# Kernel tuning notes

Measured on AMD Instinct MI355X. Metric: run time of the kernel, lower is better.

## Reference

```python
import jax, jax.numpy as jnp
import numpy as np

R = 256            # rois_per_image = cfg.TRAIN.BATCH_SIZE
FG_QUOTA = 64      # round(FG_FRACTION=0.25 * R)
FG_THRESH = 0.5
BG_HI = 0.5
BG_LO = 0.0
MEANS = jnp.array([0.0, 0.0, 0.0, 0.0], jnp.float32)
STDS = jnp.array([0.1, 0.1, 0.2, 0.2], jnp.float32)
INSIDE_W = jnp.array([1.0, 1.0, 1.0, 1.0], jnp.float32)


def _iou(boxes, gt):
    # boxes [B,M,4], gt [B,G,4] -> IoU [B,M,G]  (bbox_overlaps_batch2)
    x1 = jnp.maximum(boxes[:, :, None, 0], gt[:, None, :, 0])
    y1 = jnp.maximum(boxes[:, :, None, 1], gt[:, None, :, 1])
    x2 = jnp.minimum(boxes[:, :, None, 2], gt[:, None, :, 2])
    y2 = jnp.minimum(boxes[:, :, None, 3], gt[:, None, :, 3])
    iw = jnp.clip(x2 - x1 + 1.0, 0.0)
    ih = jnp.clip(y2 - y1 + 1.0, 0.0)
    inter = iw * ih
    area_b = (boxes[..., 2] - boxes[..., 0] + 1.0) * (boxes[..., 3] - boxes[..., 1] + 1.0)
    area_g = (gt[..., 2] - gt[..., 0] + 1.0) * (gt[..., 3] - gt[..., 1] + 1.0)
    return inter / (area_b[:, :, None] + area_g[:, None, :] - inter)


def _bbox_transform(ex, gt):
    # bbox_transform_batch2: ex,gt [B,R,4] -> targets [B,R,4]
    ew = ex[..., 2] - ex[..., 0] + 1.0
    eh = ex[..., 3] - ex[..., 1] + 1.0
    ecx = ex[..., 0] + 0.5 * ew
    ecy = ex[..., 1] + 0.5 * eh
    gw = gt[..., 2] - gt[..., 0] + 1.0
    gh = gt[..., 3] - gt[..., 1] + 1.0
    gcx = gt[..., 0] + 0.5 * gw
    gcy = gt[..., 1] + 0.5 * gh
    return jnp.stack([(gcx - ecx) / ew, (gcy - ecy) / eh,
                      jnp.log(gw / ew), jnp.log(gh / eh)], axis=-1)


def setup_inputs() -> dict:
    key = jax.random.key(0)
    B, N, G, IMG = 16, 12000, 128, 800.0
    ks = jax.random.split(key, 8)

    def boxes(k1, k2, n):
        xy = jax.random.uniform(k1, (B, n, 2)) * (IMG - 260.0)
        wh = 16.0 + jax.random.uniform(k2, (B, n, 2)) * 240.0
        return jnp.concatenate([xy, xy + wh], axis=-1)

    roi_xy = boxes(ks[0], ks[1], N)
    bidx = jnp.broadcast_to(jnp.arange(B, dtype=jnp.float32)[:, None, None], (B, N, 1))
    all_rois = jnp.concatenate([bidx, roi_xy], axis=-1)  # [B,N,5]

    gt_xy = boxes(ks[2], ks[3], G)
    gt_lab = jax.random.randint(ks[4], (B, G, 1), 1, 151).astype(jnp.float32)
    gt_boxes = jnp.concatenate([gt_xy, gt_lab], axis=-1)  # [B,G,5]
    return {"all_rois": all_rois, "gt_boxes": gt_boxes}


def reference(all_rois, gt_boxes):
    B, N, _ = all_rois.shape
    G = gt_boxes.shape[1]
    bidx = jnp.arange(B, dtype=all_rois.dtype)

    # append gt boxes as extra proposals (first col = image index)
    gt_append = jnp.concatenate(
        [jnp.broadcast_to(bidx[:, None, None], (B, G, 1)), gt_boxes[:, :, :4]], axis=2)
    rois_all = jnp.concatenate([all_rois, gt_append], axis=1)  # [B,M,5], M=N+G

    ov = _iou(rois_all[..., 1:5], gt_boxes[..., :4])  # [B,M,G]
    max_ov = ov.max(axis=2)
    gt_asgn = ov.argmax(axis=2)
    labels = jnp.take_along_axis(gt_boxes[..., 4], gt_asgn, axis=1)  # [B,M]

    fg_mask = max_ov >= FG_THRESH
    bg_mask = (max_ov < BG_HI) & (max_ov >= BG_LO)

    # deterministic random sampling via keyed top_k (replaces np.random.permutation)
    k1, k2 = jax.random.split(jax.random.key(42))
    r1 = jax.random.uniform(k1, max_ov.shape)
    r2 = jax.random.uniform(k2, max_ov.shape)
    _, fg_top = jax.lax.top_k(jnp.where(fg_mask, r1 + 2.0, r1), R)  # fg first, randomized
    _, bg_top = jax.lax.top_k(jnp.where(bg_mask, r2 + 2.0, r2), R)

    fg_num = fg_mask.sum(axis=1)
    bg_num = bg_mask.sum(axis=1)
    fg_count = jnp.minimum(fg_num, FG_QUOTA)[:, None]          # [B,1]
    bg_avail = jnp.clip(bg_num, 1, R)[:, None]
    pos = jnp.broadcast_to(jnp.arange(R)[None, :], (B, R))

    fg_pick = jnp.take_along_axis(fg_top, jnp.minimum(pos, jnp.maximum(fg_count - 1, 0)), axis=1)
    bg_pick = jnp.take_along_axis(bg_top, (pos - fg_count) % bg_avail, axis=1)
    keep = jnp.where(pos < fg_count, fg_pick, bg_pick)         # [B,R]

    lab = jnp.take_along_axis(labels, keep, axis=1)
    lab = jnp.where(pos < fg_count, lab, 0.0)                  # bg -> class 0

    rois = jnp.take_along_axis(rois_all, keep[..., None], axis=1)  # [B,R,5]
    rois = rois.at[..., 0].set(bidx[:, None])

    asgn = jnp.take_along_axis(gt_asgn, keep, axis=1)
    gt_sel = jnp.take_along_axis(gt_boxes[..., :4], asgn[..., None], axis=1)

    t = (_bbox_transform(rois[..., 1:5], gt_sel) - MEANS) / STDS
    fg4 = (lab > 0).astype(t.dtype)[..., None]
    bbox_targets = t * fg4
    inside_w = fg4 * INSIDE_W
    outside_w = (inside_w > 0).astype(t.dtype)
    return rois, lab, bbox_targets, inside_w, outside_w
```

## Files before the change

### kernel.cpp

```cpp
#include <hip/hip_runtime.h>
#include <cstdint>
#include <cstddef>


#define THREEFRY_PARTITIONABLE 1

constexpr int kB = 16;
constexpr int kN = 12000;
constexpr int kG = 128;
constexpr int kM = kN + kG;
constexpr int kM4 = kM / 4;
constexpr int kR = 256;
constexpr int kFgQuota = 64;
constexpr unsigned kSeedHi = 0u;
constexpr unsigned kSeedLo = 42u;

__device__ __forceinline__ int imin(int a, int b) { return a < b ? a : b; }
__device__ __forceinline__ int imax(int a, int b) { return a > b ? a : b; }

__device__ __forceinline__ unsigned rotl32(unsigned v, int d) {
  return (v << d) | (v >> (32 - d));
}

__device__ __forceinline__ void tf2x32(unsigned k0, unsigned k1,
                                       unsigned x0, unsigned x1,
                                       unsigned& o0, unsigned& o1) {
  const unsigned k2 = k0 ^ k1 ^ 0x1BD11BDAu;
  x0 += k0; x1 += k1;
#define TF_R(d) x0 += x1; x1 = rotl32(x1, d); x1 ^= x0;
  TF_R(13) TF_R(15) TF_R(26) TF_R(6)
  x0 += k1; x1 += k2 + 1u;
  TF_R(17) TF_R(29) TF_R(16) TF_R(24)
  x0 += k2; x1 += k0 + 2u;
  TF_R(13) TF_R(15) TF_R(26) TF_R(6)
  x0 += k0; x1 += k1 + 3u;
  TF_R(17) TF_R(29) TF_R(16) TF_R(24)
  x0 += k1; x1 += k2 + 4u;
  TF_R(13) TF_R(15) TF_R(26) TF_R(6)
  x0 += k2; x1 += k0 + 5u;
#undef TF_R
  o0 = x0; o1 = x1;
}

__device__ __forceinline__ void derive_key(int which, unsigned& ka, unsigned& kb) {
#if THREEFRY_PARTITIONABLE
  tf2x32(kSeedHi, kSeedLo, 0u, (unsigned)which, ka, kb);
#else
  unsigned a0, a1, b0, b1;
  tf2x32(kSeedHi, kSeedLo, 0u, 2u, a0, a1);
  tf2x32(kSeedHi, kSeedLo, 1u, 3u, b0, b1);
  if (which == 0) { ka = a0; kb = b0; } else { ka = a1; kb = b1; }
#endif
}

__device__ __forceinline__ float bits_to_uniform(unsigned bits) {
  return __uint_as_float((bits >> 9) | 0x3f800000u) - 1.0f;
}

__device__ __forceinline__ float jax_uniform(unsigned ka, unsigned kb, unsigned i) {
#if THREEFRY_PARTITIONABLE
  unsigned o0, o1;
  tf2x32(ka, kb, 0u, i, o0, o1);
  return bits_to_uniform(o0 ^ o1);
#else
  const unsigned H = (unsigned)(kB * kM) / 2u;
  unsigned o0, o1;
  if (i < H) { tf2x32(ka, kb, i, i + H, o0, o1); return bits_to_uniform(o0); }
  else       { tf2x32(ka, kb, i - H, i, o0, o1); return bits_to_uniform(o1); }
#endif
}

__device__ __forceinline__ unsigned mask_bin(unsigned v) {
  unsigned bn = (v - 0x40000000u) >> 11;
  return bn > 2047u ? 2047u : bn;
}

__global__ __launch_bounds__(256) void k_prep(const float* __restrict__ all_rois,
                                              const float* __restrict__ gt_boxes,
                                              unsigned* __restrict__ vb) {
  __shared__ float4 sg[kG];
  __shared__ float sga[kG];
  const int b = blockIdx.y;
  const int tid = threadIdx.x;
  if (tid < kG) {
    const float* gp = gt_boxes + ((size_t)b * kG + tid) * 5;
    const float x0 = gp[0], y0 = gp[1], x1 = gp[2], y1 = gp[3];
    sg[tid] = make_float4(x0, y0, x1, y1);
    sga[tid] = ((x1 - x0) + 1.0f) * ((y1 - y0) + 1.0f);
  }
  __syncthreads();

  const int m = blockIdx.x * 256 + tid;
  if (m >= kM) return;

  float bx0, by0, bx1, by1;
  if (m < kN) {
    const float* rp = all_rois + ((size_t)b * kN + m) * 5;
    bx0 = rp[1]; by0 = rp[2]; bx1 = rp[3]; by1 = rp[4];
  } else {
    const float4 g4 = sg[m - kN];
    bx0 = g4.x; by0 = g4.y; bx1 = g4.z; by1 = g4.w;
  }
  const float areab = ((bx1 - bx0) + 1.0f) * ((by1 - by0) + 1.0f);

  int fg = 0;
#pragma unroll 4
  for (int g = 0; g < kG; ++g) {
    const float4 g4 = sg[g];
    const float xx0 = fmaxf(bx0, g4.x);
    const float yy0 = fmaxf(by0, g4.y);
    const float xx1 = fminf(bx1, g4.z);
    const float yy1 = fminf(by1, g4.w);
    const float iw = fmaxf((xx1 - xx0) + 1.0f, 0.0f);
    const float ih = fmaxf((yy1 - yy0) + 1.0f, 0.0f);
    const float inter = iw * ih;
    const float denom = (areab + sga[g]) - inter;
    fg |= (__builtin_fmaf(-0.5f, denom, inter) >= (-0x1p-26f) * denom) ? 1 : 0;
  }

  unsigned k1a, k1b, k2a, k2b;
  derive_key(0, k1a, k1b);
  derive_key(1, k2a, k2b);
  const unsigned i = (unsigned)(b * kM + m);
  const float r1 = jax_uniform(k1a, k1b, i);
  const float r2 = jax_uniform(k2a, k2b, i);
  const float v1 = fg ? (r1 + 2.0f) : r1;
  const float v2 = fg ? r2 : (r2 + 2.0f);
  vb[(size_t)b * kM + m] = __float_as_uint(v1);
  vb[(size_t)(kB + b) * kM + m] = __float_as_uint(v2);
}

__device__ __forceinline__ int block_reduce_sum(int v, int* s_red, int tid) {
#pragma unroll
  for (int off = 32; off > 0; off >>= 1) v += __shfl_down(v, off, 64);
  __syncthreads();
  if ((tid & 63) == 0) s_red[tid >> 6] = v;
  __syncthreads();
  return s_red[0] + s_red[1] + s_red[2] + s_red[3];
}

__global__ __launch_bounds__(256) void k_select(const unsigned* __restrict__ vb,
                                                int* __restrict__ topidx,
                                                int* __restrict__ nin) {
  __shared__ int s_hist[2048];
  __shared__ unsigned long long s_cand[1024];
  __shared__ int s_scan[256];
  __shared__ int s_red[4];
  __shared__ unsigned long long s_wmax[4];
  __shared__ int s_tbin, s_cnt;

  const int which = blockIdx.x;
  const int b = blockIdx.y;
  const int tid = threadIdx.x;
  const unsigned* src = vb + (size_t)(which * kB + b) * kM;
  const uint4* src4 = (const uint4*)src;
  int* dst = topidx + (size_t)(which * kB + b) * kR;

  for (int i = tid; i < 2048; i += 256) s_hist[i] = 0;
  if (tid == 0) s_cnt = 0;
  __syncthreads();

#pragma unroll 4
  for (int i = tid; i < kM4; i += 256) {
    const uint4 u = src4[i];
#define HBIN(x) if ((x) >= 0x40000000u) atomicAdd(&s_hist[mask_bin(x)], 1);
    HBIN(u.x) HBIN(u.y) HBIN(u.z) HBIN(u.w)
#undef HBIN
  }
  __syncthreads();

  const int base = 2048 - 8 * (tid + 1);
  int s = 0;
#pragma unroll
  for (int j = 0; j < 8; ++j) s += s_hist[base + j];
  const int n_in = block_reduce_sum(s, s_red, tid);
  if (tid == 0) nin[which * kB + b] = n_in;
  const int quota = (which == 0) ? kFgQuota : kR;
  const int K = imin(n_in, quota);

  if (K == 0) {
    if (which == 0) return;
    unsigned long long best = 0ull;
    for (int m = tid; m < kM; m += 256) {
      const unsigned long long key =
          ((unsigned long long)src[m] << 32) | (unsigned)(0xFFFFFFFFu - (unsigned)m);
      if (key > best) best = key;
    }
#pragma unroll
    for (int off = 32; off > 0; off >>= 1) {
      const unsigned long long o = __shfl_down(best, off, 64);
      if (o > best) best = o;
    }
    if ((tid & 63) == 0) s_wmax[tid >> 6] = best;
    __syncthreads();
    if (tid == 0) {
      for (int w = 1; w < 4; ++w) if (s_wmax[w] > best) best = s_wmax[w];
      dst[0] = (int)(0xFFFFFFFFu - (unsigned)(best & 0xFFFFFFFFull));
    }
    return;
  }

  s_scan[tid] = s;
  __syncthreads();
  for (int off = 1; off < 256; off <<= 1) {
    const int add = (tid >= off) ? s_scan[tid - off] : 0;
    __syncthreads();
    s_scan[tid] += add;
    __syncthreads();
  }
  const int above = s_scan[tid] - s;
  int cum = above;
  for (int j = 7; j >= 0; --j) {
    const int c = s_hist[base + j];
    if (cum < K && cum + c >= K) s_tbin = base + j;
    cum += c;
  }
  __syncthreads();
  const unsigned tbin = (unsigned)s_tbin;

#pragma unroll 4
  for (int i = tid; i < kM4; i += 256) {
    const uint4 u = src4[i];
#define CAND(x, j)                                                         \
    if ((x) >= 0x40000000u && mask_bin(x) >= tbin) {                       \
      const int p = atomicAdd(&s_cnt, 1);                                  \
      if (p < 1024)                                                        \
        s_cand[p] = ((unsigned long long)(x) << 32) |                      \
                    (unsigned)(0xFFFFFFFFu - (unsigned)(4 * i + (j)));     \
    }
    CAND(u.x, 0) CAND(u.y, 1) CAND(u.z, 2) CAND(u.w, 3)
#undef CAND
  }
  __syncthreads();
  const int Nc = imin(s_cnt, 1024);

  for (int j = tid; j < Nc; j += 256) {
    const unsigned long long key = s_cand[j];
    int rank = 0;
    for (int i = 0; i < Nc; ++i) rank += (s_cand[i] > key) ? 1 : 0;
    if (rank < K)
      dst[rank] = (int)(0xFFFFFFFFu - (unsigned)(key & 0xFFFFFFFFull));
  }
}

__global__ __launch_bounds__(256) void k_final(const float* __restrict__ all_rois,
                                               const float* __restrict__ gt_boxes,
                                               const int* __restrict__ topidx,
                                               const int* __restrict__ nin,
                                               float* __restrict__ out) {
  const int lane = threadIdx.x & 63;
  const int idx = (blockIdx.x << 2) | (threadIdx.x >> 6);
  const int b = idx >> 8;
  const int pos = idx & 255;

  const int fgc = imin(nin[b], kFgQuota);
  const int bgav = imin(imax(nin[kB + b], 1), kR);
  const bool isfg = pos < fgc;
  int keep;
  if (isfg) keep = topidx[(size_t)b * kR + imin(pos, imax(fgc - 1, 0))];
  else      keep = topidx[(size_t)(kB + b) * kR + (pos - fgc) % bgav];

  const float* bp = (keep < kN) ? (all_rois + ((size_t)b * kN + keep) * 5 + 1)
                                : (gt_boxes + ((size_t)b * kG + (keep - kN)) * 5);
  const float bx0 = bp[0], by0 = bp[1], bx1 = bp[2], by1 = bp[3];
  const float areab = ((bx1 - bx0) + 1.0f) * ((by1 - by0) + 1.0f);

  unsigned long long best = 0ull;
#pragma unroll
  for (int h = 0; h < 2; ++h) {
    const int g = lane + 64 * h;
    const float* gp = gt_boxes + ((size_t)b * kG + g) * 5;
    const float gx0 = gp[0], gy0 = gp[1], gx1 = gp[2], gy1 = gp[3];
    const float ga = ((gx1 - gx0) + 1.0f) * ((gy1 - gy0) + 1.0f);
    const float xx0 = fmaxf(bx0, gx0);
    const float yy0 = fmaxf(by0, gy0);
    const float xx1 = fminf(bx1, gx1);
    const float yy1 = fminf(by1, gy1);
    const float iw = fmaxf((xx1 - xx0) + 1.0f, 0.0f);
    const float ih = fmaxf((yy1 - yy0) + 1.0f, 0.0f);
    const float inter = iw * ih;
    const float iou = inter / ((areab + ga) - inter);
    const unsigned long long key =
        ((unsigned long long)__float_as_uint(iou) << 7) | (unsigned)(127 - g);
    if (key > best) best = key;
  }
#pragma unroll
  for (int off = 1; off < 64; off <<= 1) {
    const unsigned long long o = __shfl_xor(best, off, 64);
    if (o > best) best = o;
  }
  const int a = 127 - (int)(best & 127ull);

  const float* gp = gt_boxes + ((size_t)b * kG + a) * 5;
  const float gx0 = gp[0], gy0 = gp[1], gx1 = gp[2], gy1 = gp[3];
  const float lab = isfg ? gp[4] : 0.0f;
  const float fg4 = (lab > 0.0f) ? 1.0f : 0.0f;

  const float ew = (bx1 - bx0) + 1.0f;
  const float eh = (by1 - by0) + 1.0f;
  const float ecx = bx0 + 0.5f * ew;
  const float ecy = by0 + 0.5f * eh;
  const float gw = (gx1 - gx0) + 1.0f;
  const float gh = (gy1 - gy0) + 1.0f;
  const float gcx = gx0 + 0.5f * gw;
  const float gcy = gy0 + 0.5f * gh;
  const float t0 = ((gcx - ecx) / ew) / 0.1f;
  const float t1 = ((gcy - ecy) / eh) / 0.1f;
  const float t2 = logf(gw / ew) / 0.2f;
  const float t3 = logf(gh / eh) / 0.2f;

  if (lane == 0) {
    float* o_rois = out;
    float* o_lab  = out + (size_t)kB * kR * 5;
    float* o_tgt  = o_lab + (size_t)kB * kR;
    float* o_iw   = o_tgt + (size_t)kB * kR * 4;
    float* o_ow   = o_iw  + (size_t)kB * kR * 4;
    const size_t p = (size_t)b * kR + pos;
    o_rois[p * 5 + 0] = (float)b;
    o_rois[p * 5 + 1] = bx0;
    o_rois[p * 5 + 2] = by0;
    o_rois[p * 5 + 3] = bx1;
    o_rois[p * 5 + 4] = by1;
    o_lab[p] = lab;
    o_tgt[p * 4 + 0] = t0 * fg4;
    o_tgt[p * 4 + 1] = t1 * fg4;
    o_tgt[p * 4 + 2] = t2 * fg4;
    o_tgt[p * 4 + 3] = t3 * fg4;
    o_iw[p * 4 + 0] = fg4; o_iw[p * 4 + 1] = fg4;
    o_iw[p * 4 + 2] = fg4; o_iw[p * 4 + 3] = fg4;
    o_ow[p * 4 + 0] = fg4; o_ow[p * 4 + 1] = fg4;
    o_ow[p * 4 + 2] = fg4; o_ow[p * 4 + 3] = fg4;
  }
}

extern "C" void kernel_launch(void* const* d_in, const int* in_sizes, int n_in_args,
                              void* d_out, int out_size, void* d_ws, size_t ws_size,
                              hipStream_t stream) {
  (void)in_sizes; (void)n_in_args; (void)out_size; (void)ws_size;
  const float* all_rois = (const float*)d_in[0];
  const float* gt_boxes = (const float*)d_in[1];
  float* out = (float*)d_out;

  char* ws = (char*)d_ws;
  unsigned* vb = (unsigned*)ws;
  int* topidx  = (int*)(ws + 1572864);
  int* nin     = (int*)(ws + 1572864 + 32768);

  dim3 gA((kM + 255) / 256, kB);
  k_prep<<<gA, 256, 0, stream>>>(all_rois, gt_boxes, vb);
  dim3 gB(2, kB);
  k_select<<<gB, 256, 0, stream>>>(vb, topidx, nin);
  k_final<<<1024, 256, 0, stream>>>(all_rois, gt_boxes, topidx, nin, out);
}
```

Measured before the change: 99.47 us.

## Split IoU loop across thread halves and widen select blocks to 1024 threads

k_prep now gives each ROI two threads, each testing half of the 128 GT boxes, combines the fg flag through shared memory, and has each half produce one of the two random streams. This doubles the grid and halves the per-thread serial work. k_select grows from 256 to 1024 threads per block so the histogram, candidate and rank passes over each row finish in fewer iterations, since only 32 blocks run. The cost is extra barriers, a shared-memory exchange, and more idle threads in the scan stage. derive_key is also rewritten to compute both keys and select one.

```diff
diff --git a/kernel.cpp b/kernel.cpp
--- a/kernel.cpp
+++ b/kernel.cpp
@@ -44,12 +44,17 @@
 
 __device__ __forceinline__ void derive_key(int which, unsigned& ka, unsigned& kb) {
 #if THREEFRY_PARTITIONABLE
-  tf2x32(kSeedHi, kSeedLo, 0u, (unsigned)which, ka, kb);
+  unsigned a0, a1, b0, b1;
+  tf2x32(kSeedHi, kSeedLo, 0u, 0u, a0, a1);
+  tf2x32(kSeedHi, kSeedLo, 0u, 1u, b0, b1);
+  ka = which ? b0 : a0;
+  kb = which ? b1 : a1;
 #else
   unsigned a0, a1, b0, b1;
   tf2x32(kSeedHi, kSeedLo, 0u, 2u, a0, a1);
   tf2x32(kSeedHi, kSeedLo, 1u, 3u, b0, b1);
-  if (which == 0) { ka = a0; kb = b0; } else { ka = a1; kb = b1; }
+  ka = which ? a1 : a0;
+  kb = which ? b1 : b0;
 #endif
 }
 
@@ -80,6 +85,7 @@
                                               unsigned* __restrict__ vb) {
   __shared__ float4 sg[kG];
   __shared__ float sga[kG];
+  __shared__ int s_fgp[2][128];
   const int b = blockIdx.y;
   const int tid = threadIdx.x;
   if (tid < kG) {
@@ -88,24 +94,29 @@
     sg[tid] = make_float4(x0, y0, x1, y1);
     sga[tid] = ((x1 - x0) + 1.0f) * ((y1 - y0) + 1.0f);
   }
-  __syncthreads();
-
-  const int m = blockIdx.x * 256 + tid;
-  if (m >= kM) return;
-
-  float bx0, by0, bx1, by1;
-  if (m < kN) {
-    const float* rp = all_rois + ((size_t)b * kN + m) * 5;
-    bx0 = rp[1]; by0 = rp[2]; bx1 = rp[3]; by1 = rp[4];
-  } else {
-    const float4 g4 = sg[m - kN];
-    bx0 = g4.x; by0 = g4.y; bx1 = g4.z; by1 = g4.w;
+  const int rl = tid & 127;
+  const int h = tid >> 7;
+  const int m = blockIdx.x * 128 + rl;
+  const bool valid = (m < kM);
+  __syncthreads();
+
+  float bx0 = 0.f, by0 = 0.f, bx1 = 0.f, by1 = 0.f;
+  if (valid) {
+    if (m < kN) {
+      const float* rp = all_rois + ((size_t)b * kN + m) * 5;
+      bx0 = rp[1]; by0 = rp[2]; bx1 = rp[3]; by1 = rp[4];
+    } else {
+      const float4 g4 = sg[m - kN];
+      bx0 = g4.x; by0 = g4.y; bx1 = g4.z; by1 = g4.w;
+    }
   }
   const float areab = ((bx1 - bx0) + 1.0f) * ((by1 - by0) + 1.0f);
 
-  int fg = 0;
-#pragma unroll 4
-  for (int g = 0; g < kG; ++g) {
+  int fgp = 0;
+  const int g0 = h * 64;
+#pragma unroll 8
+  for (int gg = 0; gg < 64; ++gg) {
+    const int g = g0 + gg;
     const float4 g4 = sg[g];
     const float xx0 = fmaxf(bx0, g4.x);
     const float yy0 = fmaxf(by0, g4.y);
@@ -115,38 +126,40 @@
     const float ih = fmaxf((yy1 - yy0) + 1.0f, 0.0f);
     const float inter = iw * ih;
     const float denom = (areab + sga[g]) - inter;
-    fg |= (__builtin_fmaf(-0.5f, denom, inter) >= (-0x1p-26f) * denom) ? 1 : 0;
-  }
-
-  unsigned k1a, k1b, k2a, k2b;
-  derive_key(0, k1a, k1b);
-  derive_key(1, k2a, k2b);
+    fgp |= (__builtin_fmaf(-0.5f, denom, inter) >= (-0x1p-26f) * denom) ? 1 : 0;
+  }
+  s_fgp[h][rl] = fgp;
+  __syncthreads();
+  if (!valid) return;
+  const int fg = s_fgp[0][rl] | s_fgp[1][rl];
+
+  unsigned ka, kb;
+  derive_key(h, ka, kb);
   const unsigned i = (unsigned)(b * kM + m);
-  const float r1 = jax_uniform(k1a, k1b, i);
-  const float r2 = jax_uniform(k2a, k2b, i);
-  const float v1 = fg ? (r1 + 2.0f) : r1;
-  const float v2 = fg ? r2 : (r2 + 2.0f);
-  vb[(size_t)b * kM + m] = __float_as_uint(v1);
-  vb[(size_t)(kB + b) * kM + m] = __float_as_uint(v2);
-}
-
-__device__ __forceinline__ int block_reduce_sum(int v, int* s_red, int tid) {
+  const float r = jax_uniform(ka, kb, i);
+  const float v = (fg ^ h) ? (r + 2.0f) : r;
+  vb[(size_t)(h * kB + b) * kM + m] = __float_as_uint(v);
+}
+
+__device__ __forceinline__ int block_reduce_sum_w(int v, int* s_red, int tid, int nw) {
 #pragma unroll
   for (int off = 32; off > 0; off >>= 1) v += __shfl_down(v, off, 64);
   __syncthreads();
   if ((tid & 63) == 0) s_red[tid >> 6] = v;
   __syncthreads();
-  return s_red[0] + s_red[1] + s_red[2] + s_red[3];
-}
-
-__global__ __launch_bounds__(256) void k_select(const unsigned* __restrict__ vb,
-                                                int* __restrict__ topidx,
-                                                int* __restrict__ nin) {
+  int t = 0;
+  for (int w = 0; w < nw; ++w) t += s_red[w];
+  return t;
+}
+
+__global__ __launch_bounds__(1024) void k_select(const unsigned* __restrict__ vb,
+                                                 int* __restrict__ topidx,
+                                                 int* __restrict__ nin) {
   __shared__ int s_hist[2048];
   __shared__ unsigned long long s_cand[1024];
   __shared__ int s_scan[256];
-  __shared__ int s_red[4];
-  __shared__ unsigned long long s_wmax[4];
+  __shared__ int s_red[16];
+  __shared__ unsigned long long s_wmax[16];
   __shared__ int s_tbin, s_cnt;
 
   const int which = blockIdx.x;
@@ -156,12 +169,11 @@
   const uint4* src4 = (const uint4*)src;
   int* dst = topidx + (size_t)(which * kB + b) * kR;
 
-  for (int i = tid; i < 2048; i += 256) s_hist[i] = 0;
+  for (int i = tid; i < 2048; i += 1024) s_hist[i] = 0;
   if (tid == 0) s_cnt = 0;
   __syncthreads();
 
-#pragma unroll 4
-  for (int i = tid; i < kM4; i += 256) {
+  for (int i = tid; i < kM4; i += 1024) {
     const uint4 u = src4[i];
 #define HBIN(x) if ((x) >= 0x40000000u) atomicAdd(&s_hist[mask_bin(x)], 1);
     HBIN(u.x) HBIN(u.y) HBIN(u.z) HBIN(u.w)
@@ -169,11 +181,14 @@
   }
   __syncthreads();
 
-  const int base = 2048 - 8 * (tid + 1);
   int s = 0;
-#pragma unroll
-  for (int j = 0; j < 8; ++j) s += s_hist[base + j];
-  const int n_in = block_reduce_sum(s, s_red, tid);
+  if (tid < 256) {
+    const int base = 2048 - 8 * (tid + 1);
+#pragma unroll
+    for (int j = 0; j < 8; ++j) s += s_hist[base + j];
+    s_scan[tid] = s;
+  }
+  const int n_in = block_reduce_sum_w((tid < 256) ? s : 0, s_red, tid, 16);
   if (tid == 0) nin[which * kB + b] = n_in;
   const int quota = (which == 0) ? kFgQuota : kR;
   const int K = imin(n_in, quota);
@@ -181,7 +196,7 @@
   if (K == 0) {
     if (which == 0) return;
     unsigned long long best = 0ull;
-    for (int m = tid; m < kM; m += 256) {
+    for (int m = tid; m < kM; m += 1024) {
       const unsigned long long key =
           ((unsigned long long)src[m] << 32) | (unsigned)(0xFFFFFFFFu - (unsigned)m);
       if (key > best) best = key;
@@ -191,35 +206,41 @@
       const unsigned long long o = __shfl_down(best, off, 64);
       if (o > best) best = o;
     }
+    __syncthreads();
     if ((tid & 63) == 0) s_wmax[tid >> 6] = best;
     __syncthreads();
     if (tid == 0) {
-      for (int w = 1; w < 4; ++w) if (s_wmax[w] > best) best = s_wmax[w];
+      for (int w = 1; w < 16; ++w) if (s_wmax[w] > best) best = s_wmax[w];
       dst[0] = (int)(0xFFFFFFFFu - (unsigned)(best & 0xFFFFFFFFull));
     }
     return;
   }
 
-  s_scan[tid] = s;
   __syncthreads();
   for (int off = 1; off < 256; off <<= 1) {
-    const int add = (tid >= off) ? s_scan[tid - off] : 0;
+    int add = 0;
+    if (tid < 256 && tid >= off) add = s_scan[tid - off];
     __syncthreads();
-    s_scan[tid] += add;
+    if (tid < 256) s_scan[tid] += add;
     __syncthreads();
   }
-  const int above = s_scan[tid] - s;
-  int cum = above;
-  for (int j = 7; j >= 0; --j) {
-    const int c = s_hist[base + j];
-    if (cum < K && cum + c >= K) s_tbin = base + j;
-    cum += c;
+  if (tid < 256) {
+    const int base = 2048 - 8 * (tid + 1);
+    int s2 = 0;
+#pragma unroll
+    for (int j = 0; j < 8; ++j) s2 += s_hist[base + j];
+    const int above = s_scan[tid] - s2;
+    int cum = above;
+    for (int j = 7; j >= 0; --j) {
+      const int c = s_hist[base + j];
+      if (cum < K && cum + c >= K) s_tbin = base + j;
+      cum += c;
+    }
   }
   __syncthreads();
   const unsigned tbin = (unsigned)s_tbin;
 
-#pragma unroll 4
-  for (int i = tid; i < kM4; i += 256) {
+  for (int i = tid; i < kM4; i += 1024) {
     const uint4 u = src4[i];
 #define CAND(x, j)                                                         \
     if ((x) >= 0x40000000u && mask_bin(x) >= tbin) {                       \
@@ -234,7 +255,7 @@
   __syncthreads();
   const int Nc = imin(s_cnt, 1024);
 
-  for (int j = tid; j < Nc; j += 256) {
+  for (int j = tid; j < Nc; j += 1024) {
     const unsigned long long key = s_cand[j];
     int rank = 0;
     for (int i = 0; i < Nc; ++i) rank += (s_cand[i] > key) ? 1 : 0;
@@ -346,9 +367,9 @@
   int* topidx  = (int*)(ws + 1572864);
   int* nin     = (int*)(ws + 1572864 + 32768);
 
-  dim3 gA((kM + 255) / 256, kB);
+  dim3 gA((kM + 127) / 128, kB);
   k_prep<<<gA, 256, 0, stream>>>(all_rois, gt_boxes, vb);
   dim3 gB(2, kB);
-  k_select<<<gB, 256, 0, stream>>>(vb, topidx, nin);
+  k_select<<<gB, 1024, 0, stream>>>(vb, topidx, nin);
   k_final<<<1024, 256, 0, stream>>>(all_rois, gt_boxes, topidx, nin, out);
 }
```

After: 87.50 us. 12.0% less time.
